# Kernel tuning notes

Hardware: AMD Instinct MI355X
Metric: run time of the kernel (lower is better)

Reference implementation:

```python
import jax, jax.numpy as jnp
import numpy as np

B, S, H, G, DH = 2, 2048, 16, 4, 64
D = H * DH        # 1024
DKV = G * DH      # 256
SCALE = 1.0 / np.sqrt(DH).astype(np.float32)


def apply_rope(x, rope):
    # x: [..., S, DH]; rope: [2, S, DH] (rope[0]=cos, rope[1]=sin)
    xr = x.reshape(*x.shape[:-1], DH // 2, 2)
    x_rot = jnp.stack([-xr[..., 1], xr[..., 0]], axis=-1).reshape(x.shape)
    return x * rope[0] + x_rot * rope[1]


def setup_inputs() -> dict:
    key = jax.random.key(0)
    ks = jax.random.split(key, 5)
    X = jax.random.normal(ks[0], (B, S, D), dtype=jnp.float32)
    Wq = jax.random.normal(ks[1], (D, D), dtype=jnp.float32) / np.sqrt(D).astype(np.float32)
    Wk = jax.random.normal(ks[2], (DKV, D), dtype=jnp.float32) / np.sqrt(D).astype(np.float32)
    Wv = jax.random.normal(ks[3], (DKV, D), dtype=jnp.float32) / np.sqrt(D).astype(np.float32)
    Wo = jax.random.normal(ks[4], (D, D), dtype=jnp.float32) / np.sqrt(D).astype(np.float32)
    # standard RoPE angles, interleaved (pairs (0,1),(2,3),...)
    pos = jnp.arange(S, dtype=jnp.float32)
    inv_freq = 1.0 / (10000.0 ** (jnp.arange(0, DH, 2, dtype=jnp.float32) / DH))
    ang = pos[:, None] * inv_freq[None, :]          # [S, DH/2]
    ang = jnp.repeat(ang, 2, axis=-1)               # [S, DH]
    rope = jnp.stack([jnp.cos(ang), jnp.sin(ang)])  # [2, S, DH]
    causal = jnp.tril(jnp.ones((S, S), dtype=bool))
    return {"X": X, "Wq": Wq, "Wk": Wk, "Wv": Wv, "Wo": Wo, "rope": rope, "causal": causal}


def reference(X, Wq, Wk, Wv, Wo, rope, causal):
    # QKV projections (torch Linear: y = x @ W.T)
    Q = (X @ Wq.T).reshape(B, S, H, DH).transpose(0, 2, 1, 3)   # [B,H,S,DH]
    K = (X @ Wk.T).reshape(B, S, G, DH).transpose(0, 2, 1, 3)   # [B,G,S,DH]
    V = (X @ Wv.T).reshape(B, S, G, DH).transpose(0, 2, 1, 3)   # [B,G,S,DH]
    Q = apply_rope(Q, rope)
    K = apply_rope(K, rope)
    # GQA: repeat KV heads (repeat_interleave semantics)
    K = jnp.repeat(K, H // G, axis=1)                            # [B,H,S,DH]
    V = jnp.repeat(V, H // G, axis=1)
    scores = SCALE * jnp.einsum('bhqd,bhkd->bhqk', Q, K)         # [B,H,S,S]
    scores = jnp.where(causal, scores, -jnp.inf)
    A = jax.nn.softmax(scores, axis=-1)
    Y = jnp.einsum('bhqk,bhkd->bhqd', A, V)                      # [B,H,S,DH]
    Y = Y.transpose(0, 2, 1, 3).reshape(B, S, D)
    return Y @ Wo.T
```

## Files before the change

### kernel.cpp

```cpp
#include <hip/hip_runtime.h>
#include <hip/hip_bf16.h>

#define B_   2
#define S_   2048
#define H_   16
#define G_   4
#define DH_  64
#define D_   1024
#define DKV_ 256
#define SCALE_ 0.125f
#define LDQK_ 1280

using short8  = __attribute__((ext_vector_type(8))) short;
using floatx4 = __attribute__((ext_vector_type(4))) float;
typedef unsigned short ushort_t;

__device__ __forceinline__ ushort_t f2bf(float f) {
    union { float f; unsigned u; } v; v.f = f;
    unsigned r = v.u + 0x7fffu + ((v.u >> 16) & 1u);
    return (ushort_t)(r >> 16);
}
__device__ __forceinline__ float bf2f(ushort_t u) {
    union { unsigned u; float f; } v; v.u = ((unsigned)u) << 16;
    return v.f;
}
__device__ __forceinline__ unsigned cvt_pk_bf16(float lo, float hi) {
    unsigned r;
    asm("v_cvt_pk_bf16_f32 %0, %1, %2" : "=v"(r) : "v"(lo), "v"(hi));
    return r;
}

__device__ __forceinline__ void gload16(const ushort_t* g, ushort_t* l) {
    __builtin_amdgcn_global_load_lds(
        (const __attribute__((address_space(1))) void*)g,
        (__attribute__((address_space(3))) void*)l, 16, 0, 0);
}

__global__ void pack_all(const float* __restrict__ X,  const float* __restrict__ Wq,
                         const float* __restrict__ Wk, const float* __restrict__ Wv,
                         const float* __restrict__ Wo, ushort_t* __restrict__ dst) {
    const int X4  = B_ * S_ * D_ / 4;
    const int QW4 = D_ * D_ / 4;
    const int KW4 = DKV_ * D_ / 4;
    int i = blockIdx.x * blockDim.x + threadIdx.x;
    const float* src; int off;
    if (i < X4)                        { src = X;  off = i; }
    else if (i < X4 + QW4)             { src = Wq; off = i - X4; }
    else if (i < X4 + QW4 + KW4)       { src = Wk; off = i - X4 - QW4; }
    else if (i < X4 + QW4 + 2 * KW4)   { src = Wv; off = i - X4 - QW4 - KW4; }
    else                               { src = Wo; off = i - X4 - QW4 - 2 * KW4; }
    float4 v = reinterpret_cast<const float4*>(src)[off];
    ushort4 o;
    o.x = f2bf(v.x); o.y = f2bf(v.y); o.z = f2bf(v.z); o.w = f2bf(v.w);
    reinterpret_cast<ushort4*>(dst)[i] = o;
}

__global__ __launch_bounds__(256)
void gemm_all(int mode,
              const ushort_t* __restrict__ Xb,  const ushort_t* __restrict__ Wqkb,
              const ushort_t* __restrict__ Wvb, const ushort_t* __restrict__ Wob,
              ushort_t* __restrict__ QKb, ushort_t* __restrict__ Vtb,
              const ushort_t* __restrict__ Yb, float* __restrict__ Cout,
              const float* __restrict__ rope, float qscale)
{
    __shared__ __align__(16) ushort_t Asm[2][128 * 64];
    __shared__ __align__(16) ushort_t Bsm[2][64 * 64];

    const ushort_t *Aorig, *Borig;
    ushort_t* Cb = nullptr; float* Cf = nullptr;
    int m0, n0, ldc, epi;
    if (mode == 1) {
        m0 = blockIdx.x * 128; n0 = blockIdx.y * 64;
        Aorig = Yb; Borig = Wob; Cf = Cout; ldc = D_; epi = 1;
    } else {
        const int bx = blockIdx.x;
        if (bx < 640) {
            m0 = (bx / 20) * 128; n0 = (bx % 20) * 64;
            Aorig = Xb; Borig = Wqkb; Cb = QKb; ldc = LDQK_; epi = 2;
        } else {
            const int idx = bx - 640, b = idx >> 6, rem = idx & 63;
            m0 = (rem >> 5) * 128; n0 = (rem & 31) * 64;
            Aorig = Wvb; Borig = Xb + (long)b * S_ * D_;
            Cb = Vtb + (long)b * DKV_ * S_; ldc = S_; epi = 0;
        }
    }

    const int tid = threadIdx.x, l = tid & 63, w = tid >> 6;
    const int wr = (w >> 1) * 64, wc = (w & 1) * 32;
    const int lr = l & 15, lkb = l >> 4;

    const int srow = w * 8 + (l >> 3);
    const int scol = ((l & 7) ^ ((l >> 3) & 7)) * 8;
    const ushort_t* Ast = Aorig + (long)(m0 + srow) * D_ + scol;
    const ushort_t* Bst = Borig + (long)(n0 + srow) * D_ + scol;

#define GSTAGE(buf, kt)                                                    \
    {                                                                      \
        _Pragma("unroll")                                                  \
        for (int rr = 0; rr < 4; ++rr)                                     \
            gload16(Ast + (long)rr * 32 * D_ + (kt), &Asm[buf][w * 512 + rr * 2048]); \
        _Pragma("unroll")                                                  \
        for (int c = 0; c < 2; ++c)                                        \
            gload16(Bst + (long)c * 32 * D_ + (kt), &Bsm[buf][w * 512 + c * 2048]);   \
    }

    floatx4 acc[4][2] = {};
    const int xr = (lr & 7) << 4;
    GSTAGE(0, 0);
    for (int i = 0; i < 16; ++i) {
        const int cur = i & 1;
        if (i < 15) {
            GSTAGE(cur ^ 1, (i + 1) * 64);
            asm volatile("s_waitcnt vmcnt(6)" ::: "memory");
        } else {
            asm volatile("s_waitcnt vmcnt(0)" ::: "memory");
        }
        __builtin_amdgcn_s_barrier();

#pragma unroll
        for (int ks = 0; ks < 2; ++ks) {
            short8 a[4], bb[2];
#pragma unroll
            for (int ii = 0; ii < 4; ++ii) {
                const int row = wr + ii * 16 + lr;
                a[ii] = *(const short8*)&Asm[cur][(row * 128 + ((ks * 64 + lkb * 16) ^ xr)) >> 1];
            }
#pragma unroll
            for (int j = 0; j < 2; ++j) {
                const int row = wc + j * 16 + lr;
                bb[j] = *(const short8*)&Bsm[cur][(row * 128 + ((ks * 64 + lkb * 16) ^ xr)) >> 1];
            }
            __builtin_amdgcn_s_setprio(1);
#pragma unroll
            for (int ii = 0; ii < 4; ++ii)
#pragma unroll
                for (int j = 0; j < 2; ++j)
                    acc[ii][j] = __builtin_amdgcn_mfma_f32_16x16x32_bf16(a[ii], bb[j], acc[ii][j], 0, 0, 0);
            __builtin_amdgcn_s_setprio(0);
        }
        __builtin_amdgcn_s_barrier();
    }
#undef GSTAGE

    const int rrow = lkb * 4;
#pragma unroll
    for (int i = 0; i < 4; ++i) {
#pragma unroll
        for (int j = 0; j < 2; ++j) {
#pragma unroll
            for (int r = 0; r < 4; ++r) {
                const int row = m0 + wr + i * 16 + rrow + r;
                const int col = n0 + wc + j * 16 + lr;
                if (epi == 1) {
                    Cf[(long)row * ldc + col] = acc[i][j][r];
                } else if (epi == 0) {
                    Cb[(long)row * ldc + col] = f2bf(acc[i][j][r]);
                } else {
                    const float v  = acc[i][j][r];
                    const float pv = __shfl_xor(v, 1);
                    const int   s  = row & (S_ - 1);
                    const int   d  = col & (DH_ - 1);
                    const float cc = rope[s * DH_ + d];
                    const float sn = rope[S_ * DH_ + s * DH_ + d];
                    float res = (lr & 1) ? (v * cc + pv * sn) : (v * cc - pv * sn);
                    res *= (col < D_) ? qscale : 1.0f;
                    Cb[(long)row * ldc + col] = f2bf(res);
                }
            }
        }
    }
}

__global__ __launch_bounds__(512)
void attn_kernel(const ushort_t* __restrict__ QK, const ushort_t* __restrict__ Vt,
                 ushort_t* __restrict__ Y0, ushort_t* __restrict__ Y1,
                 float* __restrict__ L0, float* __restrict__ L1)
{
    __shared__ __align__(16) ushort_t Kt [2][64 * 64];
    __shared__ __align__(16) ushort_t Vts[2][64 * 64];

    const int tid = threadIdx.x;
    const int l   = tid & 63;
    const int w   = tid >> 6;
    const int lr  = l & 15, lkb = l >> 4, lk = lkb * 8;
    const int bx = blockIdx.x, h = blockIdx.y, b = blockIdx.z;
    const int g   = h >> 2;

    const int sr  = l >> 3;
    const int sce = ((l & 7) ^ sr) * 8;
    const ushort_t* Ksrc = QK + (long)b * S_ * LDQK_ + D_ + g * DH_ + sce;
    const ushort_t* Vsrc = Vt + (long)(b * G_ + g) * DH_ * S_ + sce;

    const int rl = w * 8 + sr;
    const int kr = (rl & 0x23) | ((rl & 0x0C) << 1) | ((rl & 0x10) >> 2);

    short8 vones;
#pragma unroll
    for (int j = 0; j < 8; ++j) vones[j] = (short)0x3F80;

    for (int seg = 0; seg < 2; ++seg) {
        const int qt = seg == 0 ? (S_ / 128 - 1 - bx) : bx;
        const int t0 = seg == 0 ? qt + 1 : 0;
        const int t1 = seg == 0 ? 2 * qt + 2 : qt + 1;
        const int qrow0 = qt * 128 + w * 16;

        const ushort_t* Qp = QK + ((long)b * S_ + qrow0 + lr) * LDQK_ + h * DH_ + lk;
        const short8 bq0 = *(const short8*)(Qp);
        const short8 bq1 = *(const short8*)(Qp + 32);

        floatx4 o[4] = {};
        floatx4 osum = {};

        const ushort_t* kp = Ksrc + (long)(t0 * 64 + kr) * LDQK_;
        const ushort_t* vp = Vsrc + (long)rl * S_ + t0 * 64;

#define STAGE(buf)                                            \
    {                                                         \
        gload16(kp, &Kt[buf][w * 512]);                       \
        gload16(vp, &Vts[buf][w * 512]);                      \
        kp += 64 * LDQK_;                                     \
        vp += 64;                                             \
    }

        STAGE(0);
        asm volatile("s_waitcnt vmcnt(0)" ::: "memory");
        __builtin_amdgcn_s_barrier();

        for (int t = t0; t < t1; ++t) {
            const int cur = (t - t0) & 1;
            if (t + 1 < t1) STAGE(cur ^ 1);

            floatx4 sacc[4] = {};
            __builtin_amdgcn_s_setprio(1);
#pragma unroll
            for (int cf = 0; cf < 4; ++cf) {
                const int row = cf * 16 + lr;
                const int xr  = (row & 7) << 4;
                const short8 ak0 = *(const short8*)&Kt[cur][(row * 128 + ((lkb * 16) ^ xr)) >> 1];
                const short8 ak1 = *(const short8*)&Kt[cur][(row * 128 + ((64 + lkb * 16) ^ xr)) >> 1];
                sacc[cf] = __builtin_amdgcn_mfma_f32_16x16x32_bf16(ak0, bq0, sacc[cf], 0, 0, 0);
                sacc[cf] = __builtin_amdgcn_mfma_f32_16x16x32_bf16(ak1, bq1, sacc[cf], 0, 0, 0);
            }
            __builtin_amdgcn_s_setprio(0);

            if (t >= 2 * qt) {
                const int qg = qrow0 + lr;
#pragma unroll
                for (int cf = 0; cf < 4; ++cf) {
                    const int kvb0 = t * 64 + 32 * (cf >> 1) + 8 * lkb + 4 * (cf & 1);
#pragma unroll
                    for (int r = 0; r < 4; ++r)
                        if (kvb0 + r > qg) sacc[cf][r] = -3e38f;
                }
            }

#pragma unroll
            for (int cf = 0; cf < 4; ++cf)
#pragma unroll
                for (int r = 0; r < 4; ++r)
                    sacc[cf][r] = exp2f(sacc[cf][r]);

#pragma unroll
            for (int ks = 0; ks < 2; ++ks) {
                union { unsigned u[4]; short8 s; } pa;
#pragma unroll
                for (int j = 0; j < 4; ++j) {
                    const int cf = 2 * ks + (j >> 1);
                    const int e  = (j & 1) * 2;
                    pa.u[j] = cvt_pk_bf16(sacc[cf][e], sacc[cf][e + 1]);
                }
                __builtin_amdgcn_s_setprio(1);
#pragma unroll
                for (int df = 0; df < 4; ++df) {
                    const int vrow = df * 16 + lr;
                    const int xr   = (vrow & 7) << 4;
                    const short8 bv = *(const short8*)&Vts[cur][(vrow * 128 + ((ks * 64 + lkb * 16) ^ xr)) >> 1];
                    o[df] = __builtin_amdgcn_mfma_f32_16x16x32_bf16(pa.s, bv, o[df], 0, 0, 0);
                }
                osum = __builtin_amdgcn_mfma_f32_16x16x32_bf16(pa.s, vones, osum, 0, 0, 0);
                __builtin_amdgcn_s_setprio(0);
            }

            asm volatile("s_waitcnt vmcnt(0)" ::: "memory");
            __builtin_amdgcn_s_barrier();
        }
#undef STAGE

        ushort_t* Yp = seg == 0 ? Y1 : Y0;
        float*    Lp = seg == 0 ? L1 : L0;
#pragma unroll
        for (int r = 0; r < 4; ++r) {
            const int row = qrow0 + lkb * 4 + r;
#pragma unroll
            for (int df = 0; df < 4; ++df)
                Yp[((long)b * S_ + row) * D_ + h * DH_ + df * 16 + lr] = f2bf(o[df][r]);
            if (lr == 0)
                Lp[((long)b * S_ + row) * H_ + h] = osum[r];
        }
    }
}

__global__ void combine_kernel(ushort_t* __restrict__ Y0, const ushort_t* __restrict__ Y1,
                               const float* __restrict__ L0, const float* __restrict__ L1) {
    const int i  = blockIdx.x * blockDim.x + threadIdx.x;
    const int row = i >> 7;
    const int h   = (i & 127) >> 3;
    const float inv = 1.f / (L0[row * H_ + h] + L1[row * H_ + h]);
    const short8 y0 = ((const short8*)Y0)[i];
    const short8 y1 = ((const short8*)Y1)[i];
    union { unsigned u[4]; short8 s; } o;
#pragma unroll
    for (int j = 0; j < 4; ++j) {
        const float a = (bf2f((ushort_t)y0[2 * j])     + bf2f((ushort_t)y1[2 * j]))     * inv;
        const float c = (bf2f((ushort_t)y0[2 * j + 1]) + bf2f((ushort_t)y1[2 * j + 1])) * inv;
        o.u[j] = cvt_pk_bf16(a, c);
    }
    ((short8*)Y0)[i] = o.s;
}

extern "C" void kernel_launch(void* const* d_in, const int* in_sizes, int n_in,
                              void* d_out, int out_size, void* d_ws, size_t ws_size,
                              hipStream_t stream) {
    const float* X    = (const float*)d_in[0];
    const float* Wq   = (const float*)d_in[1];
    const float* Wk   = (const float*)d_in[2];
    const float* Wv   = (const float*)d_in[3];
    const float* Wo   = (const float*)d_in[4];
    const float* rope = (const float*)d_in[5];
    float* out = (float*)d_out;

    char* ws = (char*)d_ws;
    size_t o = 0;
    ushort_t* Xb   = (ushort_t*)(ws + o); o += (size_t)B_ * S_ * D_ * 2;
    ushort_t* Wqkb = (ushort_t*)(ws + o); o += (size_t)LDQK_ * D_ * 2;
    ushort_t* Wvb  = (ushort_t*)(ws + o); o += (size_t)DKV_ * D_ * 2;
    ushort_t* Wob  = (ushort_t*)(ws + o); o += (size_t)D_ * D_ * 2;
    ushort_t* QKb  = (ushort_t*)(ws + o); o += (size_t)B_ * S_ * LDQK_ * 2;
    ushort_t* Vtb  = (ushort_t*)(ws + o); o += (size_t)B_ * G_ * DH_ * S_ * 2;
    ushort_t* Y1b  = (ushort_t*)(ws + o); o += (size_t)B_ * S_ * D_ * 2;
    float*    L0   = (float*)(ws + o);    o += (size_t)B_ * S_ * H_ * 4;
    float*    L1   = (float*)(ws + o);    o += (size_t)B_ * S_ * H_ * 4;
    ushort_t* Y0   = Xb;

    {
        int n4 = (B_ * S_ * D_ + 2 * D_ * D_ + 2 * DKV_ * D_) / 4;
        pack_all<<<(n4 + 255) / 256, 256, 0, stream>>>(X, Wq, Wk, Wv, Wo, Xb);
    }

    const float SC2 = SCALE_ * 1.44269504f;
    gemm_all<<<dim3(768, 1, 1), 256, 0, stream>>>(
        0, Xb, Wqkb, Wvb, Wob, QKb, Vtb, nullptr, nullptr, rope, SC2);

    attn_kernel<<<dim3(S_ / 128, H_, B_), 512, 0, stream>>>(QKb, Vtb, Y0, Y1b, L0, L1);

    {
        int nthr = B_ * S_ * D_ / 8;
        combine_kernel<<<nthr / 256, 256, 0, stream>>>(Y0, Y1b, L0, L1);
    }

    gemm_all<<<dim3(32, 16, 1), 256, 0, stream>>>(
        1, Xb, Wqkb, Wvb, Wob, QKb, Vtb, Y0, out, nullptr, 0.f);
}
```

Before: 96.80 us.

## Fuse attention split-combine into output GEMM and deepen attention KV prefetch

Removes the separate combine kernel. The output-projection GEMM now loads both partial Y halves and their L sums, normalizes them in registers and writes the result into shared memory as its A operand. This saves one full read-write pass over Y and a kernel launch, but A is now loaded synchronously per K step instead of through the async global-to-LDS path. The attention kernel also goes from two to four LDS buffers, prefetching two tiles ahead and computing two tiles per barrier pair to overlap loads better, at the cost of doubled shared memory.

```diff
diff --git a/kernel.cpp b/kernel.cpp
--- a/kernel.cpp
+++ b/kernel.cpp
@@ -55,23 +55,25 @@
     reinterpret_cast<ushort4*>(dst)[i] = o;
 }
 
+template<int MODE>
 __global__ __launch_bounds__(256)
-void gemm_all(int mode,
-              const ushort_t* __restrict__ Xb,  const ushort_t* __restrict__ Wqkb,
+void gemm_all(const ushort_t* __restrict__ Xb,  const ushort_t* __restrict__ Wqkb,
               const ushort_t* __restrict__ Wvb, const ushort_t* __restrict__ Wob,
               ushort_t* __restrict__ QKb, ushort_t* __restrict__ Vtb,
-              const ushort_t* __restrict__ Yb, float* __restrict__ Cout,
+              const ushort_t* __restrict__ Y0g, const ushort_t* __restrict__ Y1g,
+              const float* __restrict__ Lg0, const float* __restrict__ Lg1,
+              float* __restrict__ Cout,
               const float* __restrict__ rope, float qscale)
 {
     __shared__ __align__(16) ushort_t Asm[2][128 * 64];
     __shared__ __align__(16) ushort_t Bsm[2][64 * 64];
 
-    const ushort_t *Aorig, *Borig;
+    const ushort_t *Aorig = nullptr, *Borig;
     ushort_t* Cb = nullptr; float* Cf = nullptr;
     int m0, n0, ldc, epi;
-    if (mode == 1) {
+    if (MODE == 1) {
         m0 = blockIdx.x * 128; n0 = blockIdx.y * 64;
-        Aorig = Yb; Borig = Wob; Cf = Cout; ldc = D_; epi = 1;
+        Borig = Wob; Cf = Cout; ldc = D_; epi = 1;
     } else {
         const int bx = blockIdx.x;
         if (bx < 640) {
@@ -91,9 +93,37 @@
 
     const int srow = w * 8 + (l >> 3);
     const int scol = ((l & 7) ^ ((l >> 3) & 7)) * 8;
-    const ushort_t* Ast = Aorig + (long)(m0 + srow) * D_ + scol;
+    const ushort_t* Ast = (MODE == 0) ? Aorig + (long)(m0 + srow) * D_ + scol : nullptr;
     const ushort_t* Bst = Borig + (long)(n0 + srow) * D_ + scol;
 
+    floatx4 acc[4][2] = {};
+    const int xr = (lr & 7) << 4;
+
+    auto do_mfma = [&](int cur) {
+#pragma unroll
+        for (int ks = 0; ks < 2; ++ks) {
+            short8 a[4], bb2[2];
+#pragma unroll
+            for (int ii = 0; ii < 4; ++ii) {
+                const int row = wr + ii * 16 + lr;
+                a[ii] = *(const short8*)&Asm[cur][(row * 128 + ((ks * 64 + lkb * 16) ^ xr)) >> 1];
+            }
+#pragma unroll
+            for (int j = 0; j < 2; ++j) {
+                const int row = wc + j * 16 + lr;
+                bb2[j] = *(const short8*)&Bsm[cur][(row * 128 + ((ks * 64 + lkb * 16) ^ xr)) >> 1];
+            }
+            __builtin_amdgcn_s_setprio(1);
+#pragma unroll
+            for (int ii = 0; ii < 4; ++ii)
+#pragma unroll
+                for (int j = 0; j < 2; ++j)
+                    acc[ii][j] = __builtin_amdgcn_mfma_f32_16x16x32_bf16(a[ii], bb2[j], acc[ii][j], 0, 0, 0);
+            __builtin_amdgcn_s_setprio(0);
+        }
+    };
+
+    if (MODE == 0) {
 #define GSTAGE(buf, kt)                                                    \
     {                                                                      \
         _Pragma("unroll")                                                  \
@@ -103,44 +133,74 @@
         for (int c = 0; c < 2; ++c)                                        \
             gload16(Bst + (long)c * 32 * D_ + (kt), &Bsm[buf][w * 512 + c * 2048]);   \
     }
-
-    floatx4 acc[4][2] = {};
-    const int xr = (lr & 7) << 4;
-    GSTAGE(0, 0);
-    for (int i = 0; i < 16; ++i) {
-        const int cur = i & 1;
-        if (i < 15) {
-            GSTAGE(cur ^ 1, (i + 1) * 64);
-            asm volatile("s_waitcnt vmcnt(6)" ::: "memory");
-        } else {
-            asm volatile("s_waitcnt vmcnt(0)" ::: "memory");
-        }
+        GSTAGE(0, 0);
+        for (int i = 0; i < 16; ++i) {
+            const int cur = i & 1;
+            if (i < 15) {
+                GSTAGE(cur ^ 1, (i + 1) * 64);
+                asm volatile("s_waitcnt vmcnt(6)" ::: "memory");
+            } else {
+                asm volatile("s_waitcnt vmcnt(0)" ::: "memory");
+            }
+            __builtin_amdgcn_s_barrier();
+            do_mfma(cur);
+            __builtin_amdgcn_s_barrier();
+        }
+#undef GSTAGE
+    } else {
+        short8 ya[4], yb[4]; float la[4];
+#define ALOAD(i2)                                                          \
+    {                                                                      \
+        _Pragma("unroll")                                                  \
+        for (int rr = 0; rr < 4; ++rr) {                                   \
+            const int arow = m0 + rr * 32 + srow;                          \
+            const long asrc = (long)arow * D_ + (i2) * 64 + scol;          \
+            ya[rr] = *(const short8*)&Y0g[asrc];                           \
+            yb[rr] = *(const short8*)&Y1g[asrc];                           \
+            la[rr] = Lg0[arow * H_ + (i2)] + Lg1[arow * H_ + (i2)];        \
+        }                                                                  \
+    }
+#define AWRITE(buf)                                                        \
+    {                                                                      \
+        _Pragma("unroll")                                                  \
+        for (int rr = 0; rr < 4; ++rr) {                                   \
+            const float inv = 1.f / la[rr];                                \
+            union { unsigned u[4]; short8 s; } pk;                         \
+            _Pragma("unroll")                                              \
+            for (int j = 0; j < 4; ++j) {                                  \
+                const float a0 = (bf2f((ushort_t)ya[rr][2*j])   + bf2f((ushort_t)yb[rr][2*j]))   * inv; \
+                const float a1 = (bf2f((ushort_t)ya[rr][2*j+1]) + bf2f((ushort_t)yb[rr][2*j+1])) * inv; \
+                pk.u[j] = cvt_pk_bf16(a0, a1);                             \
+            }                                                              \
+            *(short8*)&Asm[buf][w * 512 + rr * 2048 + l * 8] = pk.s;       \
+        }                                                                  \
+    }
+#define BSTG(buf, i2)                                                      \
+    {                                                                      \
+        _Pragma("unroll")                                                  \
+        for (int c = 0; c < 2; ++c)                                        \
+            gload16(Bst + (long)c * 32 * D_ + (i2) * 64, &Bsm[buf][w * 512 + c * 2048]); \
+    }
+        ALOAD(0); BSTG(0, 0);
+        asm volatile("s_waitcnt vmcnt(0)" ::: "memory");
+        AWRITE(0);
+        asm volatile("s_waitcnt lgkmcnt(0)" ::: "memory");
         __builtin_amdgcn_s_barrier();
-
-#pragma unroll
-        for (int ks = 0; ks < 2; ++ks) {
-            short8 a[4], bb[2];
-#pragma unroll
-            for (int ii = 0; ii < 4; ++ii) {
-                const int row = wr + ii * 16 + lr;
-                a[ii] = *(const short8*)&Asm[cur][(row * 128 + ((ks * 64 + lkb * 16) ^ xr)) >> 1];
-            }
-#pragma unroll
-            for (int j = 0; j < 2; ++j) {
-                const int row = wc + j * 16 + lr;
-                bb[j] = *(const short8*)&Bsm[cur][(row * 128 + ((ks * 64 + lkb * 16) ^ xr)) >> 1];
-            }
-            __builtin_amdgcn_s_setprio(1);
-#pragma unroll
-            for (int ii = 0; ii < 4; ++ii)
-#pragma unroll
-                for (int j = 0; j < 2; ++j)
-                    acc[ii][j] = __builtin_amdgcn_mfma_f32_16x16x32_bf16(a[ii], bb[j], acc[ii][j], 0, 0, 0);
-            __builtin_amdgcn_s_setprio(0);
-        }
-        __builtin_amdgcn_s_barrier();
-    }
-#undef GSTAGE
+        for (int i = 0; i < 16; ++i) {
+            const int cur = i & 1;
+            if (i < 15) { ALOAD(i + 1); BSTG(cur ^ 1, i + 1); }
+            do_mfma(cur);
+            if (i < 15) {
+                asm volatile("s_waitcnt vmcnt(0)" ::: "memory");
+                AWRITE(cur ^ 1);
+                asm volatile("s_waitcnt lgkmcnt(0)" ::: "memory");
+            }
+            __builtin_amdgcn_s_barrier();
+        }
+#undef ALOAD
+#undef AWRITE
+#undef BSTG
+    }
 
     const int rrow = lkb * 4;
 #pragma unroll
@@ -176,8 +236,8 @@
                  ushort_t* __restrict__ Y0, ushort_t* __restrict__ Y1,
                  float* __restrict__ L0, float* __restrict__ L1)
 {
-    __shared__ __align__(16) ushort_t Kt [2][64 * 64];
-    __shared__ __align__(16) ushort_t Vts[2][64 * 64];
+    __shared__ __align__(16) ushort_t Kt [4][64 * 64];
+    __shared__ __align__(16) ushort_t Vts[4][64 * 64];
 
     const int tid = threadIdx.x;
     const int l   = tid & 63;
@@ -198,10 +258,17 @@
 #pragma unroll
     for (int j = 0; j < 8; ++j) vones[j] = (short)0x3F80;
 
+#define STG(bi, tt)                                                       \
+    {                                                                     \
+        gload16(Ksrc + (long)((tt) * 64 + kr) * LDQK_, &Kt[bi][w * 512]); \
+        gload16(Vsrc + (long)rl * S_ + (tt) * 64,      &Vts[bi][w * 512]);\
+    }
+
     for (int seg = 0; seg < 2; ++seg) {
         const int qt = seg == 0 ? (S_ / 128 - 1 - bx) : bx;
         const int t0 = seg == 0 ? qt + 1 : 0;
-        const int t1 = seg == 0 ? 2 * qt + 2 : qt + 1;
+        const int n  = qt + 1;
+        const int tmax = t0 + n - 1;
         const int qrow0 = qt * 128 + w * 16;
 
         const ushort_t* Qp = QK + ((long)b * S_ + qrow0 + lr) * LDQK_ + h * DH_ + lk;
@@ -211,25 +278,7 @@
         floatx4 o[4] = {};
         floatx4 osum = {};
 
-        const ushort_t* kp = Ksrc + (long)(t0 * 64 + kr) * LDQK_;
-        const ushort_t* vp = Vsrc + (long)rl * S_ + t0 * 64;
-
-#define STAGE(buf)                                            \
-    {                                                         \
-        gload16(kp, &Kt[buf][w * 512]);                       \
-        gload16(vp, &Vts[buf][w * 512]);                      \
-        kp += 64 * LDQK_;                                     \
-        vp += 64;                                             \
-    }
-
-        STAGE(0);
-        asm volatile("s_waitcnt vmcnt(0)" ::: "memory");
-        __builtin_amdgcn_s_barrier();
-
-        for (int t = t0; t < t1; ++t) {
-            const int cur = (t - t0) & 1;
-            if (t + 1 < t1) STAGE(cur ^ 1);
-
+        auto compute_tile = [&](int cur, int t) {
             floatx4 sacc[4] = {};
             __builtin_amdgcn_s_setprio(1);
 #pragma unroll
@@ -280,11 +329,23 @@
                 osum = __builtin_amdgcn_mfma_f32_16x16x32_bf16(pa.s, vones, osum, 0, 0, 0);
                 __builtin_amdgcn_s_setprio(0);
             }
-
-            asm volatile("s_waitcnt vmcnt(0)" ::: "memory");
+        };
+
+        STG(0, t0);
+        STG(1, (t0 + 1 <= tmax) ? t0 + 1 : tmax);
+
+        for (int i = 0; i < n; i += 2) {
+            const int tn2 = (t0 + i + 2 <= tmax) ? t0 + i + 2 : tmax;
+            const int tn3 = (t0 + i + 3 <= tmax) ? t0 + i + 3 : tmax;
+            STG((i + 2) & 3, tn2);
+            STG((i + 3) & 3, tn3);
+            asm volatile("s_waitcnt vmcnt(4)" ::: "memory");
             __builtin_amdgcn_s_barrier();
-        }
-#undef STAGE
+            compute_tile(i & 3, t0 + i);
+            if (i + 1 < n) compute_tile((i + 1) & 3, t0 + i + 1);
+            __builtin_amdgcn_s_barrier();
+        }
+        asm volatile("s_waitcnt vmcnt(0)" ::: "memory");
 
         ushort_t* Yp = seg == 0 ? Y1 : Y0;
         float*    Lp = seg == 0 ? L1 : L0;
@@ -297,25 +358,9 @@
             if (lr == 0)
                 Lp[((long)b * S_ + row) * H_ + h] = osum[r];
         }
-    }
-}
-
-__global__ void combine_kernel(ushort_t* __restrict__ Y0, const ushort_t* __restrict__ Y1,
-                               const float* __restrict__ L0, const float* __restrict__ L1) {
-    const int i  = blockIdx.x * blockDim.x + threadIdx.x;
-    const int row = i >> 7;
-    const int h   = (i & 127) >> 3;
-    const float inv = 1.f / (L0[row * H_ + h] + L1[row * H_ + h]);
-    const short8 y0 = ((const short8*)Y0)[i];
-    const short8 y1 = ((const short8*)Y1)[i];
-    union { unsigned u[4]; short8 s; } o;
-#pragma unroll
-    for (int j = 0; j < 4; ++j) {
-        const float a = (bf2f((ushort_t)y0[2 * j])     + bf2f((ushort_t)y1[2 * j]))     * inv;
-        const float c = (bf2f((ushort_t)y0[2 * j + 1]) + bf2f((ushort_t)y1[2 * j + 1])) * inv;
-        o.u[j] = cvt_pk_bf16(a, c);
-    }
-    ((short8*)Y0)[i] = o.s;
+        __builtin_amdgcn_s_barrier();
+    }
+#undef STG
 }
 
 extern "C" void kernel_launch(void* const* d_in, const int* in_sizes, int n_in,
@@ -348,16 +393,12 @@
     }
 
     const float SC2 = SCALE_ * 1.44269504f;
-    gemm_all<<<dim3(768, 1, 1), 256, 0, stream>>>(
-        0, Xb, Wqkb, Wvb, Wob, QKb, Vtb, nullptr, nullptr, rope, SC2);
+    gemm_all<0><<<dim3(768, 1, 1), 256, 0, stream>>>(
+        Xb, Wqkb, Wvb, Wob, QKb, Vtb, nullptr, nullptr, nullptr, nullptr,
+        nullptr, rope, SC2);
 
     attn_kernel<<<dim3(S_ / 128, H_, B_), 512, 0, stream>>>(QKb, Vtb, Y0, Y1b, L0, L1);
 
-    {
-        int nthr = B_ * S_ * D_ / 8;
-        combine_kernel<<<nthr / 256, 256, 0, stream>>>(Y0, Y1b, L0, L1);
-    }
-
-    gemm_all<<<dim3(32, 16, 1), 256, 0, stream>>>(
-        1, Xb, Wqkb, Wvb, Wob, QKb, Vtb, Y0, out, nullptr, 0.f);
-}
+    gemm_all<1><<<dim3(32, 16, 1), 256, 0, stream>>>(
+        Xb, Wqkb, Wvb, Wob, QKb, Vtb, Y0, Y1b, L0, L1, out, nullptr, 0.f);
+}
```

Result: slower. 102.9 us (+6.3%).

## Deepen attention KV pipeline to four buffers and template GEMM mode

Applied to the files above, without the earlier changes.

The attention kernel now keeps four K/V tile buffers in shared memory and processes two tiles per barrier interval. It prefetches two tiles ahead and waits with a partial vmcnt, which halves the number of barriers and overlaps global loads with more compute. Past the end of the range it issues redundant clamped loads. The GEMM kernel's mode becomes a template parameter, so the mode branch is resolved at compile time. The cost is doubled LDS use per block (64KB), which may reduce occupancy, plus an extra barrier between segments.

```diff
diff --git a/kernel.cpp b/kernel.cpp
--- a/kernel.cpp
+++ b/kernel.cpp
@@ -55,9 +55,9 @@
     reinterpret_cast<ushort4*>(dst)[i] = o;
 }
 
+template<int MODE>
 __global__ __launch_bounds__(256)
-void gemm_all(int mode,
-              const ushort_t* __restrict__ Xb,  const ushort_t* __restrict__ Wqkb,
+void gemm_all(const ushort_t* __restrict__ Xb,  const ushort_t* __restrict__ Wqkb,
               const ushort_t* __restrict__ Wvb, const ushort_t* __restrict__ Wob,
               ushort_t* __restrict__ QKb, ushort_t* __restrict__ Vtb,
               const ushort_t* __restrict__ Yb, float* __restrict__ Cout,
@@ -69,7 +69,7 @@
     const ushort_t *Aorig, *Borig;
     ushort_t* Cb = nullptr; float* Cf = nullptr;
     int m0, n0, ldc, epi;
-    if (mode == 1) {
+    if (MODE == 1) {
         m0 = blockIdx.x * 128; n0 = blockIdx.y * 64;
         Aorig = Yb; Borig = Wob; Cf = Cout; ldc = D_; epi = 1;
     } else {
@@ -176,8 +176,8 @@
                  ushort_t* __restrict__ Y0, ushort_t* __restrict__ Y1,
                  float* __restrict__ L0, float* __restrict__ L1)
 {
-    __shared__ __align__(16) ushort_t Kt [2][64 * 64];
-    __shared__ __align__(16) ushort_t Vts[2][64 * 64];
+    __shared__ __align__(16) ushort_t Kt [4][64 * 64];
+    __shared__ __align__(16) ushort_t Vts[4][64 * 64];
 
     const int tid = threadIdx.x;
     const int l   = tid & 63;
@@ -198,10 +198,17 @@
 #pragma unroll
     for (int j = 0; j < 8; ++j) vones[j] = (short)0x3F80;
 
+#define STG(bi, tt)                                                       \
+    {                                                                     \
+        gload16(Ksrc + (long)((tt) * 64 + kr) * LDQK_, &Kt[bi][w * 512]); \
+        gload16(Vsrc + (long)rl * S_ + (tt) * 64,      &Vts[bi][w * 512]);\
+    }
+
     for (int seg = 0; seg < 2; ++seg) {
         const int qt = seg == 0 ? (S_ / 128 - 1 - bx) : bx;
         const int t0 = seg == 0 ? qt + 1 : 0;
-        const int t1 = seg == 0 ? 2 * qt + 2 : qt + 1;
+        const int n  = qt + 1;
+        const int tmax = t0 + n - 1;
         const int qrow0 = qt * 128 + w * 16;
 
         const ushort_t* Qp = QK + ((long)b * S_ + qrow0 + lr) * LDQK_ + h * DH_ + lk;
@@ -211,25 +218,7 @@
         floatx4 o[4] = {};
         floatx4 osum = {};
 
-        const ushort_t* kp = Ksrc + (long)(t0 * 64 + kr) * LDQK_;
-        const ushort_t* vp = Vsrc + (long)rl * S_ + t0 * 64;
-
-#define STAGE(buf)                                            \
-    {                                                         \
-        gload16(kp, &Kt[buf][w * 512]);                       \
-        gload16(vp, &Vts[buf][w * 512]);                      \
-        kp += 64 * LDQK_;                                     \
-        vp += 64;                                             \
-    }
-
-        STAGE(0);
-        asm volatile("s_waitcnt vmcnt(0)" ::: "memory");
-        __builtin_amdgcn_s_barrier();
-
-        for (int t = t0; t < t1; ++t) {
-            const int cur = (t - t0) & 1;
-            if (t + 1 < t1) STAGE(cur ^ 1);
-
+        auto compute_tile = [&](int cur, int t) {
             floatx4 sacc[4] = {};
             __builtin_amdgcn_s_setprio(1);
 #pragma unroll
@@ -280,11 +269,23 @@
                 osum = __builtin_amdgcn_mfma_f32_16x16x32_bf16(pa.s, vones, osum, 0, 0, 0);
                 __builtin_amdgcn_s_setprio(0);
             }
-
-            asm volatile("s_waitcnt vmcnt(0)" ::: "memory");
+        };
+
+        STG(0, t0);
+        STG(1, (t0 + 1 <= tmax) ? t0 + 1 : tmax);
+
+        for (int i = 0; i < n; i += 2) {
+            const int tn2 = (t0 + i + 2 <= tmax) ? t0 + i + 2 : tmax;
+            const int tn3 = (t0 + i + 3 <= tmax) ? t0 + i + 3 : tmax;
+            STG((i + 2) & 3, tn2);
+            STG((i + 3) & 3, tn3);
+            asm volatile("s_waitcnt vmcnt(4)" ::: "memory");
             __builtin_amdgcn_s_barrier();
-        }
-#undef STAGE
+            compute_tile(i & 3, t0 + i);
+            if (i + 1 < n) compute_tile((i + 1) & 3, t0 + i + 1);
+            __builtin_amdgcn_s_barrier();
+        }
+        asm volatile("s_waitcnt vmcnt(0)" ::: "memory");
 
         ushort_t* Yp = seg == 0 ? Y1 : Y0;
         float*    Lp = seg == 0 ? L1 : L0;
@@ -297,7 +298,9 @@
             if (lr == 0)
                 Lp[((long)b * S_ + row) * H_ + h] = osum[r];
         }
-    }
+        __builtin_amdgcn_s_barrier();
+    }
+#undef STG
 }
 
 __global__ void combine_kernel(ushort_t* __restrict__ Y0, const ushort_t* __restrict__ Y1,
@@ -348,8 +351,8 @@
     }
 
     const float SC2 = SCALE_ * 1.44269504f;
-    gemm_all<<<dim3(768, 1, 1), 256, 0, stream>>>(
-        0, Xb, Wqkb, Wvb, Wob, QKb, Vtb, nullptr, nullptr, rope, SC2);
+    gemm_all<0><<<dim3(768, 1, 1), 256, 0, stream>>>(
+        Xb, Wqkb, Wvb, Wob, QKb, Vtb, nullptr, nullptr, rope, SC2);
 
     attn_kernel<<<dim3(S_ / 128, H_, B_), 512, 0, stream>>>(QKb, Vtb, Y0, Y1b, L0, L1);
 
@@ -358,6 +361,6 @@
         combine_kernel<<<nthr / 256, 256, 0, stream>>>(Y0, Y1b, L0, L1);
     }
 
-    gemm_all<<<dim3(32, 16, 1), 256, 0, stream>>>(
-        1, Xb, Wqkb, Wvb, Wob, QKb, Vtb, Y0, out, nullptr, 0.f);
-}
+    gemm_all<1><<<dim3(32, 16, 1), 256, 0, stream>>>(
+        Xb, Wqkb, Wvb, Wob, QKb, Vtb, Y0, out, nullptr, 0.f);
+}
```

Measured after the change: 96.32 us. No clear change (-0.5%).
